# Performance work log

Hardware: AMD Instinct MI355X
Metric: run time of the kernel (lower is better)

The kernel has to match this reference:

```python
import jax, jax.numpy as jnp
import numpy as np

B, D, H, W_, C = 2, 64, 64, 64, 96
EPS = 1e-5


def _merge(t):
    # t: [b, d, h, w, c] -> [b, d/2, h/2, w/2, 8*c], channel blocks ordered
    # by itertools.product(i, j, k): block index = i*4 + j*2 + k.
    b, d, h, w, c = t.shape
    t = t.reshape(b, d // 2, 2, h // 2, 2, w // 2, 2, c)
    t = t.transpose(0, 1, 3, 5, 2, 4, 6, 7)  # i slowest, then j, then k
    return t.reshape(b, d // 2, h // 2, w // 2, 8 * c)


def setup_inputs() -> dict:
    key = jax.random.key(0)
    k1, k2, k3 = jax.random.split(key, 3)
    x = jax.random.normal(k1, (B, D, H, W_, C), dtype=jnp.float32)
    mask = jax.random.bernoulli(k2, 0.7, (B, D, H, W_, 1)).astype(jnp.float32)
    gamma = jnp.ones((8 * C,), dtype=jnp.float32)
    beta = jnp.zeros((8 * C,), dtype=jnp.float32)
    W = (jax.random.normal(k3, (8 * C, 2 * C), dtype=jnp.float32)
         / np.float32(np.sqrt(8 * C)))  # Linear(8*dim, 2*dim, bias=False), stored [in, out]
    return {"x": x, "mask": mask, "gamma": gamma, "beta": beta, "W": W}


def reference(x, mask, gamma, beta, W):
    xm = x * mask  # broadcast of [b,d,h,w,1] mask over channels
    xr = _merge(xm)            # [b, d/2, h/2, w/2, 8c]
    mr = _merge(mask)          # [b, d/2, h/2, w/2, 8]
    mask_out = mr.sum(axis=-1) > 0
    # LayerNorm over last (8c) dim, biased variance, eps=1e-5
    mu = xr.mean(axis=-1, keepdims=True)
    var = jnp.mean(jnp.square(xr - mu), axis=-1, keepdims=True)
    xn = (xr - mu) * jax.lax.rsqrt(var + EPS) * gamma + beta
    out = jnp.einsum('bdhwc,co->bdhwo', xn, W)  # [b, d/2, h/2, w/2, 2*dim]
    return out, mask_out
```

## Files before the change

kernel.cpp:

```cpp
#include <hip/hip_runtime.h>

#define NOUT 192
#define M_TOTAL 65536
#define OUT0 (M_TOTAL * NOUT)

typedef __attribute__((ext_vector_type(8))) short  short8;
typedef __attribute__((ext_vector_type(4))) float  f32x4;

__device__ __forceinline__ unsigned short f2bf(float f) {
    union { float f; unsigned u; } a; a.f = f;
    unsigned r = a.u + 0x7FFFu + ((a.u >> 16) & 1u);
    return (unsigned short)(r >> 16);
}

__device__ __forceinline__ void gload16(void* lds, const void* g) {
    __builtin_amdgcn_global_load_lds((const __attribute__((address_space(1))) void*)g,
                                     (__attribute__((address_space(3))) void*)lds, 16, 0, 0);
}

__global__ __launch_bounds__(256) void prepw_kernel(const float* __restrict__ Wm,
                                                    const float* __restrict__ gamma,
                                                    unsigned short* __restrict__ Wb) {
    int t = blockIdx.x * 256 + threadIdx.x;
    if (t >= 24 * 12 * 512) return;
    int e  = t & 7;
    int l  = (t >> 3) & 63;
    int f  = t >> 9;
    int fn = f % 12;
    int ks = f / 12;
    int k  = ks * 32 + ((l >> 4) << 3) + e;
    Wb[t] = f2bf(gamma[k] * Wm[k * NOUT + fn * 16 + (l & 15)]);
}

__global__ __launch_bounds__(256) void prepuv_kernel(const float* __restrict__ Wm,
                                                     const float* __restrict__ gamma,
                                                     const float* __restrict__ beta,
                                                     float2* __restrict__ uv) {
    __shared__ float2 red[4];
    const int o = blockIdx.x, tid = threadIdx.x;
    float u = 0.f, v = 0.f;
    for (int c = tid; c < 768; c += 256) {
        const float w = Wm[c * NOUT + o];
        u = fmaf(gamma[c], w, u);
        v = fmaf(beta[c],  w, v);
    }
#pragma unroll
    for (int off = 32; off >= 1; off >>= 1) {
        u += __shfl_xor(u, off);
        v += __shfl_xor(v, off);
    }
    if ((tid & 63) == 0) red[tid >> 6] = make_float2(u, v);
    __syncthreads();
    if (tid == 0) {
        float2 a = red[0];
        a.x += red[1].x + red[2].x + red[3].x;
        a.y += red[1].y + red[2].y + red[3].y;
        uv[o] = a;
    }
}

__global__ __launch_bounds__(256) void fused_kernel(
    const float* __restrict__ x, const float* __restrict__ mask,
    const unsigned short* __restrict__ Wb, const float2* __restrict__ uv,
    float* __restrict__ out)
{
    __shared__ __align__(16) char Blds[3 * 12288];

    const int tid = threadIdx.x, l = tid & 63, wv = tid >> 6;
    const int lr = l & 15, q = l >> 4, q8 = q << 3;
    const int rowbase = blockIdx.x << 6;
    const int rg = rowbase + wv * 16 + lr;
    const int w2 = rg & 31, h2 = (rg >> 5) & 31, d2 = (rg >> 10) & 31, b = rg >> 15;
    const int vbase = ((b * 64 + d2 * 2) * 64 + h2 * 2) * 64 + w2 * 2;
    const int vb96 = vbase * 96;

    float mk[8];
#pragma unroll
    for (int t = 0; t < 8; ++t)
        mk[t] = mask[vbase + ((t >> 2) << 12) + (((t >> 1) & 1) << 6) + (t & 1)];

    float mo = fmaxf(fmaxf(fmaxf(mk[0], mk[1]), fmaxf(mk[2], mk[3])),
                     fmaxf(fmaxf(mk[4], mk[5]), fmaxf(mk[6], mk[7])));
    if (q == 0) out[OUT0 + rg] = (mo > 0.f) ? 1.f : 0.f;

    f32x4 acc[12] = {};
    float s = 0.f, s2 = 0.f;
    float4 a0, a1;

    {
        const float* p = x + vb96 + q8;
        a0 = *(const float4*)p;
        a1 = *(const float4*)(p + 4);
#pragma unroll
        for (int c = 0; c < 3; ++c)
            gload16(Blds + (c * 256 + tid) * 16, Wb + (size_t)(c * 256 + tid) * 8);
    }

#pragma unroll
    for (int ks = 0; ks < 24; ++ks) {
        const float mkv = mk[ks / 3];
        float4 u0 = a0, u1 = a1;
        u0.x *= mkv; u0.y *= mkv; u0.z *= mkv; u0.w *= mkv;
        u1.x *= mkv; u1.y *= mkv; u1.z *= mkv; u1.w *= mkv;
        s  += (u0.x + u0.y) + (u0.z + u0.w) + (u1.x + u1.y) + (u1.z + u1.w);
        s2 += (u0.x*u0.x + u0.y*u0.y) + (u0.z*u0.z + u0.w*u0.w)
            + (u1.x*u1.x + u1.y*u1.y) + (u1.z*u1.z + u1.w*u1.w);
        short8 fa;
        fa[0] = (short)f2bf(u0.x); fa[1] = (short)f2bf(u0.y);
        fa[2] = (short)f2bf(u0.z); fa[3] = (short)f2bf(u0.w);
        fa[4] = (short)f2bf(u1.x); fa[5] = (short)f2bf(u1.y);
        fa[6] = (short)f2bf(u1.z); fa[7] = (short)f2bf(u1.w);

        if (ks < 23) {
            const int kn = ks + 1;
            const int bi = kn / 3;
            const int voff96 = (((bi >> 2) << 12) + (((bi >> 1) & 1) << 6) + (bi & 1)) * 96;
            const float* p = x + vb96 + voff96 + (kn % 3) * 32 + q8;
            a0 = *(const float4*)p;
            a1 = *(const float4*)(p + 4);
            const unsigned short* ws = Wb + (size_t)kn * 6144;
            char* bd = Blds + (kn % 3) * 12288;
#pragma unroll
            for (int c = 0; c < 3; ++c)
                gload16(bd + (c * 256 + tid) * 16, ws + (size_t)(c * 256 + tid) * 8);
            asm volatile("s_waitcnt vmcnt(5)" ::: "memory");
        } else {
            asm volatile("s_waitcnt vmcnt(0)" ::: "memory");
        }
        __builtin_amdgcn_s_barrier();

        const char* bb = Blds + (ks % 3) * 12288 + l * 16;
#pragma unroll
        for (int fn = 0; fn < 12; ++fn) {
            const short8 bf = *(const short8*)(bb + fn * 1024);
            acc[fn] = __builtin_amdgcn_mfma_f32_16x16x32_bf16(fa, bf, acc[fn], 0, 0, 0);
        }
    }

    s  += __shfl_xor(s, 16);  s  += __shfl_xor(s, 32);
    s2 += __shfl_xor(s2, 16); s2 += __shfl_xor(s2, 32);
    const float mu   = s * (1.f / 768.f);
    const float var  = s2 * (1.f / 768.f) - mu * mu;
    const float rs   = rsqrtf(var + 1e-5f);
    const float murs = mu * rs;

    float2 uvv[12];
#pragma unroll
    for (int fn = 0; fn < 12; ++fn) uvv[fn] = uv[fn * 16 + lr];

#pragma unroll
    for (int j = 0; j < 4; ++j) {
        const int rowD = (q << 2) + j;
        const float rsj   = __shfl(rs,   rowD);
        const float mursj = __shfl(murs, rowD);
        float* orow = out + (size_t)(rowbase + wv * 16 + rowD) * NOUT;
#pragma unroll
        for (int fn = 0; fn < 12; ++fn)
            orow[fn * 16 + lr] = fmaf(rsj, acc[fn][j], fmaf(-mursj, uvv[fn].x, uvv[fn].y));
    }
}

extern "C" void kernel_launch(void* const* d_in, const int* in_sizes, int n_in,
                              void* d_out, int out_size, void* d_ws, size_t ws_size,
                              hipStream_t stream) {
    const float* x     = (const float*)d_in[0];
    const float* mask  = (const float*)d_in[1];
    const float* gamma = (const float*)d_in[2];
    const float* beta  = (const float*)d_in[3];
    const float* Wm    = (const float*)d_in[4];
    float* out = (float*)d_out;

    unsigned short* Wb  = (unsigned short*)d_ws;
    float2*         uvp = (float2*)((char*)d_ws + 294912);

    prepw_kernel <<<576,  256, 0, stream>>>(Wm, gamma, Wb);
    prepuv_kernel<<<192,  256, 0, stream>>>(Wm, gamma, beta, uvp);
    fused_kernel <<<1024, 256, 0, stream>>>(x, mask, Wb, uvp, out);
}
```

Before: 84.45 us.

## Stage activation tiles in LDS and split output columns across waves

The fused kernel now loads each 16-row activation tile (and its mask) into double-buffered, XOR-swizzled LDS with async global-to-LDS loads. The 192 output columns are split so each wave computes 48 columns for the same 16 rows, with W fragments read directly from global/L2 instead of LDS. Each block processes four tiles in a pipelined loop, prefetching two tiles ahead. This is meant to coalesce x loads and overlap them with compute. In exchange, every wave re-reads the W fragments from global memory, the large LDS footprint limits occupancy to one block, and the vmcnt wait counts are fragile.

```diff
diff --git a/kernel.cpp b/kernel.cpp
--- a/kernel.cpp
+++ b/kernel.cpp
@@ -3,6 +3,8 @@
 #define NOUT 192
 #define M_TOTAL 65536
 #define OUT0 (M_TOTAL * NOUT)
+#define CHUNK 12288
+#define TILE_LDS (4 * CHUNK + 1024)
 
 typedef __attribute__((ext_vector_type(8))) short  short8;
 typedef __attribute__((ext_vector_type(4))) float  f32x4;
@@ -59,104 +61,134 @@
     }
 }
 
-__global__ __launch_bounds__(256) void fused_kernel(
+__global__ __launch_bounds__(256, 1) void fused_kernel(
     const float* __restrict__ x, const float* __restrict__ mask,
     const unsigned short* __restrict__ Wb, const float2* __restrict__ uv,
     float* __restrict__ out)
 {
-    __shared__ __align__(16) char Blds[3 * 12288];
+    __shared__ __align__(16) char raw[2 * TILE_LDS];
 
     const int tid = threadIdx.x, l = tid & 63, wv = tid >> 6;
-    const int lr = l & 15, q = l >> 4, q8 = q << 3;
-    const int rowbase = blockIdx.x << 6;
-    const int rg = rowbase + wv * 16 + lr;
-    const int w2 = rg & 31, h2 = (rg >> 5) & 31, d2 = (rg >> 10) & 31, b = rg >> 15;
-    const int vbase = ((b * 64 + d2 * 2) * 64 + h2 * 2) * 64 + w2 * 2;
-    const int vb96 = vbase * 96;
-
-    float mk[8];
-#pragma unroll
-    for (int t = 0; t < 8; ++t)
-        mk[t] = mask[vbase + ((t >> 2) << 12) + (((t >> 1) & 1) << 6) + (t & 1)];
-
-    float mo = fmaxf(fmaxf(fmaxf(mk[0], mk[1]), fmaxf(mk[2], mk[3])),
-                     fmaxf(fmaxf(mk[4], mk[5]), fmaxf(mk[6], mk[7])));
-    if (q == 0) out[OUT0 + rg] = (mo > 0.f) ? 1.f : 0.f;
-
-    f32x4 acc[12] = {};
-    float s = 0.f, s2 = 0.f;
-    float4 a0, a1;
-
-    {
-        const float* p = x + vb96 + q8;
-        a0 = *(const float4*)p;
-        a1 = *(const float4*)(p + 4);
-#pragma unroll
-        for (int c = 0; c < 3; ++c)
-            gload16(Blds + (c * 256 + tid) * 16, Wb + (size_t)(c * 256 + tid) * 8);
-    }
-
-#pragma unroll
-    for (int ks = 0; ks < 24; ++ks) {
-        const float mkv = mk[ks / 3];
-        float4 u0 = a0, u1 = a1;
-        u0.x *= mkv; u0.y *= mkv; u0.z *= mkv; u0.w *= mkv;
-        u1.x *= mkv; u1.y *= mkv; u1.z *= mkv; u1.w *= mkv;
-        s  += (u0.x + u0.y) + (u0.z + u0.w) + (u1.x + u1.y) + (u1.z + u1.w);
-        s2 += (u0.x*u0.x + u0.y*u0.y) + (u0.z*u0.z + u0.w*u0.w)
-            + (u1.x*u1.x + u1.y*u1.y) + (u1.z*u1.z + u1.w*u1.w);
-        short8 fa;
-        fa[0] = (short)f2bf(u0.x); fa[1] = (short)f2bf(u0.y);
-        fa[2] = (short)f2bf(u0.z); fa[3] = (short)f2bf(u0.w);
-        fa[4] = (short)f2bf(u1.x); fa[5] = (short)f2bf(u1.y);
-        fa[6] = (short)f2bf(u1.z); fa[7] = (short)f2bf(u1.w);
-
-        if (ks < 23) {
-            const int kn = ks + 1;
-            const int bi = kn / 3;
-            const int voff96 = (((bi >> 2) << 12) + (((bi >> 1) & 1) << 6) + (bi & 1)) * 96;
-            const float* p = x + vb96 + voff96 + (kn % 3) * 32 + q8;
-            a0 = *(const float4*)p;
-            a1 = *(const float4*)(p + 4);
-            const unsigned short* ws = Wb + (size_t)kn * 6144;
-            char* bd = Blds + (kn % 3) * 12288;
+    const int lr = l & 15, q = l >> 4;
+    const int T0 = blockIdx.x << 2;
+    const int fxor = (lr >> 1) & 7;
+
+    float2 uvv[3];
+#pragma unroll
+    for (int c = 0; c < 3; ++c) uvv[c] = uv[wv * 48 + c * 16 + lr];
+
+    int gsrco[12];
+#pragma unroll
+    for (int ld = 0; ld < 12; ++ld) {
+        const int s = (ld << 6) + l;
+        gsrco[ld] = (s ^ (((s / 24) >> 2) & 7)) << 4;
+    }
+
+    const short8* Wv = (const short8*)Wb;
+    const int bbase = wv * 192 + l;
+
+    auto issue_tile = [&](int T, int bb) {
+        const int rgb = T << 4;
+        const int w2b = (T & 1) << 4;
+        const int h2 = (rgb >> 5) & 31, d2 = (rgb >> 10) & 31, b = rgb >> 15;
+        const int d = (d2 << 1) + (wv >> 1), h = (h2 << 1) + (wv & 1);
+        const char* gsrc = (const char*)(x +
+            ((((size_t)b * 64 + d) * 64 + h) * 64 + ((size_t)w2b << 1)) * 96);
+        char* ldsb = raw + bb * TILE_LDS + wv * CHUNK;
+#pragma unroll
+        for (int ld = 0; ld < 12; ++ld)
+            gload16(ldsb + (ld << 10), gsrc + gsrco[ld]);
+        if (wv == 0) {
+            const int ij = l >> 4;
+            const int dm = (d2 << 1) + (ij >> 1), hm = (h2 << 1) + (ij & 1);
+            const char* msrc = (const char*)(mask +
+                (((size_t)b * 64 + dm) * 64 + hm) * 64 + ((l & 15) << 2));
+            gload16(raw + bb * TILE_LDS + 4 * CHUNK, msrc);
+        }
+    };
+
+    issue_tile(T0 + 0, 0);
+    issue_tile(T0 + 1, 1);
+    asm volatile("s_waitcnt vmcnt(12)" ::: "memory");
+    __builtin_amdgcn_sched_barrier(0);
+    __builtin_amdgcn_s_barrier();
+    __builtin_amdgcn_sched_barrier(0);
+
+    int cur = 0;
+#pragma unroll 1
+    for (int t = 0; t < 4; ++t) {
+        const int T = T0 + t;
+        const char* cb = raw + cur * TILE_LDS;
+        const float* ml = (const float*)(cb + 4 * CHUNK);
+
+        const int wmo = (T & 1) << 5;
+        float mk[8];
+#pragma unroll
+        for (int bi = 0; bi < 8; ++bi)
+            mk[bi] = ml[(bi >> 1) * 64 + wmo + (lr << 1) + (bi & 1)];
+
+        f32x4 acc[3] = {};
+        float s = 0.f, s2 = 0.f;
+#pragma unroll
+        for (int ks = 0; ks < 24; ++ks) {
+            const int bi = ks / 3, m = ks % 3;
+            const int u16 = ((lr << 1) + (bi & 1)) * 24 + (m << 3) + (q << 1);
+            const char* ap = cb + (bi >> 1) * CHUNK;
+            const float4 r0 = *(const float4*)(ap + ((u16 ^ fxor) << 4));
+            const float4 r1 = *(const float4*)(ap + (((u16 + 1) ^ fxor) << 4));
+            const float mkv = mk[bi];
+            const float u0x = r0.x * mkv, u0y = r0.y * mkv, u0z = r0.z * mkv, u0w = r0.w * mkv;
+            const float u1x = r1.x * mkv, u1y = r1.y * mkv, u1z = r1.z * mkv, u1w = r1.w * mkv;
+            s  += (u0x + u0y) + (u0z + u0w) + (u1x + u1y) + (u1z + u1w);
+            s2 += (u0x*u0x + u0y*u0y) + (u0z*u0z + u0w*u0w)
+                + (u1x*u1x + u1y*u1y) + (u1z*u1z + u1w*u1w);
+            short8 fa;
+            fa[0] = (short)f2bf(u0x); fa[1] = (short)f2bf(u0y);
+            fa[2] = (short)f2bf(u0z); fa[3] = (short)f2bf(u0w);
+            fa[4] = (short)f2bf(u1x); fa[5] = (short)f2bf(u1y);
+            fa[6] = (short)f2bf(u1z); fa[7] = (short)f2bf(u1w);
+            const short8 b0 = Wv[ks * 768 + bbase];
+            const short8 b1 = Wv[ks * 768 + bbase + 64];
+            const short8 b2 = Wv[ks * 768 + bbase + 128];
+            acc[0] = __builtin_amdgcn_mfma_f32_16x16x32_bf16(fa, b0, acc[0], 0, 0, 0);
+            acc[1] = __builtin_amdgcn_mfma_f32_16x16x32_bf16(fa, b1, acc[1], 0, 0, 0);
+            acc[2] = __builtin_amdgcn_mfma_f32_16x16x32_bf16(fa, b2, acc[2], 0, 0, 0);
+        }
+
+        __builtin_amdgcn_s_barrier();
+        __builtin_amdgcn_sched_barrier(0);
+        if (t + 2 < 4) issue_tile(T + 2, cur);
+
+        s  += __shfl_xor(s, 16);  s  += __shfl_xor(s, 32);
+        s2 += __shfl_xor(s2, 16); s2 += __shfl_xor(s2, 32);
+        const float mu   = s * (1.f / 768.f);
+        const float var  = s2 * (1.f / 768.f) - mu * mu;
+        const float rs   = rsqrtf(var + 1e-5f);
+        const float murs = mu * rs;
+#pragma unroll
+        for (int j = 0; j < 4; ++j) {
+            const int row = (q << 2) + j;
+            const float rsj   = __shfl(rs,   row);
+            const float mursj = __shfl(murs, row);
+            float* orow = out + (size_t)((T << 4) + row) * NOUT;
 #pragma unroll
             for (int c = 0; c < 3; ++c)
-                gload16(bd + (c * 256 + tid) * 16, ws + (size_t)(c * 256 + tid) * 8);
-            asm volatile("s_waitcnt vmcnt(5)" ::: "memory");
-        } else {
-            asm volatile("s_waitcnt vmcnt(0)" ::: "memory");
-        }
-        __builtin_amdgcn_s_barrier();
-
-        const char* bb = Blds + (ks % 3) * 12288 + l * 16;
-#pragma unroll
-        for (int fn = 0; fn < 12; ++fn) {
-            const short8 bf = *(const short8*)(bb + fn * 1024);
-            acc[fn] = __builtin_amdgcn_mfma_f32_16x16x32_bf16(fa, bf, acc[fn], 0, 0, 0);
-        }
-    }
-
-    s  += __shfl_xor(s, 16);  s  += __shfl_xor(s, 32);
-    s2 += __shfl_xor(s2, 16); s2 += __shfl_xor(s2, 32);
-    const float mu   = s * (1.f / 768.f);
-    const float var  = s2 * (1.f / 768.f) - mu * mu;
-    const float rs   = rsqrtf(var + 1e-5f);
-    const float murs = mu * rs;
-
-    float2 uvv[12];
-#pragma unroll
-    for (int fn = 0; fn < 12; ++fn) uvv[fn] = uv[fn * 16 + lr];
-
-#pragma unroll
-    for (int j = 0; j < 4; ++j) {
-        const int rowD = (q << 2) + j;
-        const float rsj   = __shfl(rs,   rowD);
-        const float mursj = __shfl(murs, rowD);
-        float* orow = out + (size_t)(rowbase + wv * 16 + rowD) * NOUT;
-#pragma unroll
-        for (int fn = 0; fn < 12; ++fn)
-            orow[fn * 16 + lr] = fmaf(rsj, acc[fn][j], fmaf(-mursj, uvv[fn].x, uvv[fn].y));
+                orow[wv * 48 + c * 16 + lr] =
+                    fmaf(rsj, acc[c][j], fmaf(-mursj, uvv[c].x, uvv[c].y));
+        }
+        if (wv == 0 && q == 0) {
+            const float mo = fmaxf(fmaxf(fmaxf(mk[0], mk[1]), fmaxf(mk[2], mk[3])),
+                                   fmaxf(fmaxf(mk[4], mk[5]), fmaxf(mk[6], mk[7])));
+            out[OUT0 + (T << 4) + lr] = (mo > 0.f) ? 1.f : 0.f;
+        }
+
+        if (t < 3) {
+            asm volatile("s_waitcnt vmcnt(24)" ::: "memory");
+            __builtin_amdgcn_sched_barrier(0);
+            __builtin_amdgcn_s_barrier();
+            __builtin_amdgcn_sched_barrier(0);
+        }
+        cur ^= 1;
     }
 }
 
```

New measurement: 258.2 us. 206% more time.
